# Optimization experiments

Measured on AMD Instinct MI355X. Metric: run time of the kernel, lower is better.

## Reference

```python
import jax, jax.numpy as jnp
import numpy as np

COUT, CIN = 1024, 1024  # self.shape = (cout, cin) in the torch module
NNZ = 131072


def setup_inputs() -> dict:
    key = jax.random.key(0)
    k_x, k_v, k_r, k_c = jax.random.split(key, 4)
    x = jax.random.normal(k_x, (4, 4096, CIN), dtype=jnp.float32)
    values = jax.random.normal(k_v, (NNZ,), dtype=jnp.float32)
    rows = jax.random.randint(k_r, (NNZ,), 0, COUT, dtype=jnp.int32)
    cols = jax.random.randint(k_c, (NNZ,), 0, CIN, dtype=jnp.int32)
    indices = jnp.stack([rows, cols], axis=0)  # [2, nnz], integer-valued
    return {"x": x, "values": values, "indices": indices}


def reference(x, values, indices):
    # torch: sparse_coo_tensor(indices, values, (cout, cin)).coalesce();
    # coalescing sums duplicate (row, col) entries -> scatter-add densify.
    rows, cols = indices[0], indices[1]
    W = jnp.zeros((COUT, CIN), dtype=values.dtype).at[rows, cols].add(values)
    # 3D path: out[b, l, co] = sum_ci W[co, ci] * x[b, l, ci]
    return jnp.einsum('blc,oc->blo', x, W)
```

## Files before the change

### kernel.cpp

```cpp
#include <hip/hip_runtime.h>
#include <cstdint>
#include <cstddef>

#define CIN  1024
#define COUT 1024

typedef __attribute__((ext_vector_type(8))) short bf16x8;
typedef __attribute__((ext_vector_type(4))) float f32x4;

__device__ __forceinline__ unsigned short f2bf(float f) {
    union { float f; unsigned int i; } v;
    v.f = f;
    unsigned int u = v.i;
    u += 0x7FFFu + ((u >> 16) & 1u);
    return (unsigned short)(u >> 16);
}

__device__ __forceinline__ void cvt8(const float* __restrict__ s,
                                     unsigned short* __restrict__ d) {
    float4 v0 = *(const float4*)s;
    float4 v1 = *(const float4*)(s + 4);
    union { bf16x8 v; unsigned short u[8]; } w;
    w.u[0] = f2bf(v0.x); w.u[1] = f2bf(v0.y); w.u[2] = f2bf(v0.z); w.u[3] = f2bf(v0.w);
    w.u[4] = f2bf(v1.x); w.u[5] = f2bf(v1.y); w.u[6] = f2bf(v1.z); w.u[7] = f2bf(v1.w);
    *(bf16x8*)d = w.v;
}

__global__ void zero_f32(float4* __restrict__ p) {
    p[blockIdx.x * 256 + threadIdx.x] = float4{0.f, 0.f, 0.f, 0.f};
}

__global__ void scatter_cvtx(const float* __restrict__ vals,
                             const int* __restrict__ rows,
                             const int* __restrict__ cols,
                             float* __restrict__ W, int nnz, int nsb,
                             const float* __restrict__ x,
                             unsigned short* __restrict__ Xb) {
    const int b = blockIdx.x;
    if (b < nsb) {
        const int i = b * 256 + threadIdx.x;
        if (i < nnz) atomicAdd(W + (size_t)rows[i] * CIN + cols[i], vals[i]);
    } else {
        const size_t i = (((size_t)(b - nsb) * 256) + threadIdx.x) * 8;
        cvt8(x + i, Xb + i);
    }
}

__global__ void cvt_bf16_bulk(const float* __restrict__ src, unsigned short* __restrict__ dst) {
    size_t i = ((size_t)blockIdx.x * 256 + threadIdx.x) * 8;
    cvt8(src + i, dst + i);
}


#define GLD16(SRC_, DST_)                                                     \
  __builtin_amdgcn_global_load_lds(                                           \
      (const __attribute__((address_space(1))) void*)(SRC_),                  \
      (__attribute__((address_space(3))) void*)(DST_), 16, 0, 0)

#define STAGE_A(BUF_, HALF_, KT_) do {                                        \
    GLD16(pa + (size_t)((HALF_) * 128)      * CIN + (size_t)(KT_) * 64,       \
          As + (BUF_) * 16384 + ((HALF_) * 128) * 64 + tid8);                 \
    GLD16(pa + (size_t)((HALF_) * 128 + 64) * CIN + (size_t)(KT_) * 64,       \
          As + (BUF_) * 16384 + ((HALF_) * 128 + 64) * 64 + tid8);            \
  } while (0)

#define STAGE_B(BUF_, HALF_, KT_) do {                                        \
    GLD16(pb + (size_t)((HALF_) * 128)      * CIN + (size_t)(KT_) * 64,       \
          Bs + (BUF_) * 16384 + ((HALF_) * 128) * 64 + tid8);                 \
    GLD16(pb + (size_t)((HALF_) * 128 + 64) * CIN + (size_t)(KT_) * 64,       \
          Bs + (BUF_) * 16384 + ((HALF_) * 128 + 64) * 64 + tid8);            \
  } while (0)

#define LOAD_A(BUF_, QA_) do {                                                \
    const unsigned short* ab_ = As + (BUF_) * 16384 + ((QA_) * 128 + wm64) * 64; \
    _Pragma("unroll")                                                         \
    for (int ks_ = 0; ks_ < 2; ++ks_) {                                       \
      const int cx_ = ((ks_ * 4 + quad) ^ s7) * 8;                            \
      _Pragma("unroll")                                                       \
      for (int mf_ = 0; mf_ < 4; ++mf_)                                       \
        af[ks_][mf_] = *(const bf16x8*)(ab_ + (mf_ * 16 + l16) * 64 + cx_);   \
    }                                                                         \
  } while (0)

#define LOAD_B(BUF_, QB_, DST_) do {                                          \
    const unsigned short* bb_ = Bs + (BUF_) * 16384 + ((QB_) * 128 + wn32) * 64; \
    _Pragma("unroll")                                                         \
    for (int ks_ = 0; ks_ < 2; ++ks_) {                                       \
      const int cx_ = ((ks_ * 4 + quad) ^ s7) * 8;                            \
      _Pragma("unroll")                                                       \
      for (int nf_ = 0; nf_ < 2; ++nf_)                                       \
        DST_[ks_][nf_] = *(const bf16x8*)(bb_ + (nf_ * 16 + l16) * 64 + cx_); \
    }                                                                         \
  } while (0)

#define MFMA_Q(QA_, QB_, BF_)                                                 \
    _Pragma("unroll")                                                         \
    for (int ks_ = 0; ks_ < 2; ++ks_)                                         \
      _Pragma("unroll")                                                       \
      for (int mf_ = 0; mf_ < 4; ++mf_)                                       \
        _Pragma("unroll")                                                     \
        for (int nf_ = 0; nf_ < 2; ++nf_)                                     \
          acc[QA_][QB_][mf_][nf_] = __builtin_amdgcn_mfma_f32_16x16x32_bf16(  \
              af[ks_][mf_], BF_[ks_][nf_], acc[QA_][QB_][mf_][nf_], 0, 0, 0)

#define WRITE_CQ(QA_, QB_) do {                                               \
    _Pragma("unroll")                                                         \
    for (int mf_ = 0; mf_ < 4; ++mf_)                                         \
      _Pragma("unroll")                                                       \
      for (int nf_ = 0; nf_ < 2; ++nf_) {                                     \
        const int row0_ = rowA0 + (QA_) * 128 + wm64 + mf_ * 16 + quad * 4;   \
        float* cp_ = C + (size_t)row0_ * COUT                                 \
                       + rowB0 + (QB_) * 128 + wn32 + nf_ * 16 + l16;         \
        _Pragma("unroll")                                                     \
        for (int r_ = 0; r_ < 4; ++r_)                                        \
            cp_[(size_t)r_ * COUT] = acc[QA_][QB_][mf_][nf_][r_];             \
      }                                                                       \
  } while (0)

#define SYNC_PRE() do {                                                       \
    __builtin_amdgcn_s_barrier();                                             \
    __builtin_amdgcn_s_setprio(1);                                            \
  } while (0)

#define SYNC_POST() __builtin_amdgcn_s_setprio(0)

__global__ __launch_bounds__(512, 2) void gemm_8ph_v4(
    const unsigned short* __restrict__ A,
    const unsigned short* __restrict__ B,
    float* __restrict__ C,
    int M) {
    (void)M;
    constexpr int K = CIN;

    __shared__ __align__(16) unsigned short As[2 * 16384];
    __shared__ __align__(16) unsigned short Bs[2 * 16384];

    const int tid  = threadIdx.x;
    const int lane = tid & 63;
    const int w    = tid >> 6;
    const int quad = lane >> 4;
    const int l16  = lane & 15;
    const int s7   = l16 & 7;
    const int wm64 = (w >> 2) * 64;
    const int wn32 = (w & 3) * 32;

    const int rowA0 = blockIdx.x * 256;
    const int rowB0 = blockIdx.y * 256;

    const int stg_row = tid >> 3;
    const int c_data  = (tid & 7) ^ (stg_row & 7);
    const int tid8    = tid * 8;
    const unsigned short* pa = A + (size_t)(rowA0 + stg_row) * K + c_data * 8;
    const unsigned short* pb = B + (size_t)(rowB0 + stg_row) * K + c_data * 8;

    f32x4 acc[2][2][4][2] = {};

    STAGE_A(0, 0, 0); STAGE_B(0, 0, 0); STAGE_B(0, 1, 0); STAGE_A(0, 1, 0);
    STAGE_A(1, 0, 1); STAGE_B(1, 0, 1);
    asm volatile("s_waitcnt vmcnt(4)" ::: "memory");
    __builtin_amdgcn_s_barrier();

#pragma unroll 1
    for (int i = 0; i < 7; ++i) {
        const int k1 = 2 * i + 1;
        const int k2 = 2 * i + 2;
        const int k3 = 2 * i + 3;

        bf16x8 af[2][4];
        bf16x8 bf0[2][2], bf1[2][2];

        LOAD_A(0, 0); LOAD_B(0, 0, bf0);
        STAGE_B(1, 1, k1);
        SYNC_PRE(); MFMA_Q(0, 0, bf0); SYNC_POST();
        __builtin_amdgcn_s_barrier();

        LOAD_B(0, 1, bf1);
        STAGE_A(1, 1, k1);
        SYNC_PRE(); MFMA_Q(0, 1, bf1); SYNC_POST();
        __builtin_amdgcn_s_barrier();

        LOAD_A(0, 1);
        STAGE_A(0, 0, k2);
        SYNC_PRE(); MFMA_Q(1, 0, bf0); SYNC_POST();
        __builtin_amdgcn_s_barrier();

        STAGE_B(0, 0, k2);
        SYNC_PRE(); MFMA_Q(1, 1, bf1); SYNC_POST();
        asm volatile("s_waitcnt vmcnt(4)" ::: "memory");
        __builtin_amdgcn_s_barrier();

        LOAD_A(1, 0); LOAD_B(1, 0, bf0);
        STAGE_B(0, 1, k2);
        SYNC_PRE(); MFMA_Q(0, 0, bf0); SYNC_POST();
        __builtin_amdgcn_s_barrier();

        LOAD_B(1, 1, bf1);
        STAGE_A(0, 1, k2);
        SYNC_PRE(); MFMA_Q(0, 1, bf1); SYNC_POST();
        __builtin_amdgcn_s_barrier();

        LOAD_A(1, 1);
        STAGE_A(1, 0, k3);
        SYNC_PRE(); MFMA_Q(1, 0, bf0); SYNC_POST();
        __builtin_amdgcn_s_barrier();

        STAGE_B(1, 0, k3);
        SYNC_PRE(); MFMA_Q(1, 1, bf1); SYNC_POST();
        asm volatile("s_waitcnt vmcnt(4)" ::: "memory");
        __builtin_amdgcn_s_barrier();
    }

    {
        bf16x8 af[2][4];
        bf16x8 bf0[2][2], bf1[2][2];

        LOAD_A(0, 0); LOAD_B(0, 0, bf0);
        STAGE_B(1, 1, 15);
        SYNC_PRE(); MFMA_Q(0, 0, bf0); SYNC_POST();
        __builtin_amdgcn_s_barrier();

        LOAD_B(0, 1, bf1);
        STAGE_A(1, 1, 15);
        SYNC_PRE(); MFMA_Q(0, 1, bf1); SYNC_POST();
        __builtin_amdgcn_s_barrier();

        LOAD_A(0, 1);
        SYNC_PRE(); MFMA_Q(1, 0, bf0); SYNC_POST();
        __builtin_amdgcn_s_barrier();

        SYNC_PRE(); MFMA_Q(1, 1, bf1); SYNC_POST();
        asm volatile("s_waitcnt vmcnt(0)" ::: "memory");
        __builtin_amdgcn_s_barrier();

        LOAD_A(1, 0); LOAD_B(1, 0, bf0); LOAD_B(1, 1, bf1);
        __builtin_amdgcn_s_setprio(1); MFMA_Q(0, 0, bf0); __builtin_amdgcn_s_setprio(0);
        WRITE_CQ(0, 0);

        __builtin_amdgcn_s_setprio(1); MFMA_Q(0, 1, bf1); __builtin_amdgcn_s_setprio(0);
        WRITE_CQ(0, 1);

        LOAD_A(1, 1);
        __builtin_amdgcn_s_setprio(1); MFMA_Q(1, 0, bf0); __builtin_amdgcn_s_setprio(0);
        WRITE_CQ(1, 0);

        __builtin_amdgcn_s_setprio(1); MFMA_Q(1, 1, bf1); __builtin_amdgcn_s_setprio(0);
        WRITE_CQ(1, 1);
    }
}

extern "C" void kernel_launch(void* const* d_in, const int* in_sizes, int n_in,
                              void* d_out, int out_size, void* d_ws, size_t ws_size,
                              hipStream_t stream) {
    const float* x    = (const float*)d_in[0];
    const float* vals = (const float*)d_in[1];
    const int*   idx  = (const int*)d_in[2];

    float* out = (float*)d_out;

    const int nnz = in_sizes[2] / 2;
    const int M   = in_sizes[0] / CIN;

    const size_t wf_bytes = (size_t)COUT * CIN * sizeof(float);
    const size_t wb_bytes = (size_t)COUT * CIN * sizeof(unsigned short);

    float*          Wf = (float*)d_ws;
    unsigned short* Wb = (unsigned short*)((char*)d_ws + wf_bytes);
    unsigned short* Xb = (unsigned short*)((char*)d_ws + wf_bytes + wb_bytes);

    const int nsb = (nnz + 255) / 256;
    const unsigned cvtx_blocks = (unsigned)((size_t)M * CIN / (256 * 8));

    zero_f32<<<dim3(COUT * CIN / (256 * 4)), dim3(256), 0, stream>>>((float4*)Wf);
    scatter_cvtx<<<dim3((unsigned)nsb + cvtx_blocks), dim3(256), 0, stream>>>(
        vals, idx, idx + nnz, Wf, nnz, nsb, x, Xb);
    cvt_bf16_bulk<<<dim3(COUT * CIN / (256 * 8)), dim3(256), 0, stream>>>(Wf, Wb);
    gemm_8ph_v4<<<dim3(M / 256, COUT / 256), dim3(512), 0, stream>>>(Xb, Wb, out, M);
}
```

Baseline: 155.0 us.

## Replace eight-phase interleaved GEMM pipeline with simple two-barrier double buffering

```diff
diff --git a/kernel.cpp b/kernel.cpp
--- a/kernel.cpp
+++ b/kernel.cpp
@@ -71,6 +71,11 @@
           Bs + (BUF_) * 16384 + ((HALF_) * 128 + 64) * 64 + tid8);            \
   } while (0)
 
+#define STAGE_TILE(BUF_, KT_) do {                                            \
+    STAGE_A(BUF_, 0, KT_); STAGE_A(BUF_, 1, KT_);                             \
+    STAGE_B(BUF_, 0, KT_); STAGE_B(BUF_, 1, KT_);                             \
+  } while (0)
+
 #define LOAD_A(BUF_, QA_) do {                                                \
     const unsigned short* ab_ = As + (BUF_) * 16384 + ((QA_) * 128 + wm64) * 64; \
     _Pragma("unroll")                                                         \
@@ -102,6 +107,19 @@
         for (int nf_ = 0; nf_ < 2; ++nf_)                                     \
           acc[QA_][QB_][mf_][nf_] = __builtin_amdgcn_mfma_f32_16x16x32_bf16(  \
               af[ks_][mf_], BF_[ks_][nf_], acc[QA_][QB_][mf_][nf_], 0, 0, 0)
+
+#define TILE_COMPUTE(BUF_) do {                                               \
+    bf16x8 af[2][4];                                                          \
+    bf16x8 bf0[2][2], bf1[2][2];                                              \
+    LOAD_A(BUF_, 0); LOAD_B(BUF_, 0, bf0); LOAD_B(BUF_, 1, bf1);              \
+    __builtin_amdgcn_s_setprio(1);                                            \
+    MFMA_Q(0, 0, bf0); MFMA_Q(0, 1, bf1);                                     \
+    __builtin_amdgcn_s_setprio(0);                                            \
+    LOAD_A(BUF_, 1);                                                          \
+    __builtin_amdgcn_s_setprio(1);                                            \
+    MFMA_Q(1, 0, bf0); MFMA_Q(1, 1, bf1);                                     \
+    __builtin_amdgcn_s_setprio(0);                                            \
+  } while (0)
 
 #define WRITE_CQ(QA_, QB_) do {                                               \
     _Pragma("unroll")                                                         \
@@ -117,14 +135,7 @@
       }                                                                       \
   } while (0)
 
-#define SYNC_PRE() do {                                                       \
-    __builtin_amdgcn_s_barrier();                                             \
-    __builtin_amdgcn_s_setprio(1);                                            \
-  } while (0)
-
-#define SYNC_POST() __builtin_amdgcn_s_setprio(0)
-
-__global__ __launch_bounds__(512, 2) void gemm_8ph_v4(
+__global__ __launch_bounds__(512, 2) void gemm_2bar(
     const unsigned short* __restrict__ A,
     const unsigned short* __restrict__ B,
     float* __restrict__ C,
@@ -155,83 +166,32 @@
 
     f32x4 acc[2][2][4][2] = {};
 
-    STAGE_A(0, 0, 0); STAGE_B(0, 0, 0); STAGE_B(0, 1, 0); STAGE_A(0, 1, 0);
-    STAGE_A(1, 0, 1); STAGE_B(1, 0, 1);
-    asm volatile("s_waitcnt vmcnt(4)" ::: "memory");
+    STAGE_TILE(0, 0);
+    STAGE_TILE(1, 1);
+    asm volatile("s_waitcnt vmcnt(8)" ::: "memory");
     __builtin_amdgcn_s_barrier();
 
 #pragma unroll 1
     for (int i = 0; i < 7; ++i) {
-        const int k1 = 2 * i + 1;
-        const int k2 = 2 * i + 2;
-        const int k3 = 2 * i + 3;
-
-        bf16x8 af[2][4];
-        bf16x8 bf0[2][2], bf1[2][2];
-
-        LOAD_A(0, 0); LOAD_B(0, 0, bf0);
-        STAGE_B(1, 1, k1);
-        SYNC_PRE(); MFMA_Q(0, 0, bf0); SYNC_POST();
-        __builtin_amdgcn_s_barrier();
-
-        LOAD_B(0, 1, bf1);
-        STAGE_A(1, 1, k1);
-        SYNC_PRE(); MFMA_Q(0, 1, bf1); SYNC_POST();
-        __builtin_amdgcn_s_barrier();
-
-        LOAD_A(0, 1);
-        STAGE_A(0, 0, k2);
-        SYNC_PRE(); MFMA_Q(1, 0, bf0); SYNC_POST();
-        __builtin_amdgcn_s_barrier();
-
-        STAGE_B(0, 0, k2);
-        SYNC_PRE(); MFMA_Q(1, 1, bf1); SYNC_POST();
-        asm volatile("s_waitcnt vmcnt(4)" ::: "memory");
-        __builtin_amdgcn_s_barrier();
-
-        LOAD_A(1, 0); LOAD_B(1, 0, bf0);
-        STAGE_B(0, 1, k2);
-        SYNC_PRE(); MFMA_Q(0, 0, bf0); SYNC_POST();
-        __builtin_amdgcn_s_barrier();
-
-        LOAD_B(1, 1, bf1);
-        STAGE_A(0, 1, k2);
-        SYNC_PRE(); MFMA_Q(0, 1, bf1); SYNC_POST();
-        __builtin_amdgcn_s_barrier();
-
-        LOAD_A(1, 1);
-        STAGE_A(1, 0, k3);
-        SYNC_PRE(); MFMA_Q(1, 0, bf0); SYNC_POST();
-        __builtin_amdgcn_s_barrier();
-
-        STAGE_B(1, 0, k3);
-        SYNC_PRE(); MFMA_Q(1, 1, bf1); SYNC_POST();
-        asm volatile("s_waitcnt vmcnt(4)" ::: "memory");
+        TILE_COMPUTE(0);
+        __builtin_amdgcn_s_barrier();
+        STAGE_TILE(0, 2 * i + 2);
+        asm volatile("s_waitcnt vmcnt(8)" ::: "memory");
+        __builtin_amdgcn_s_barrier();
+        TILE_COMPUTE(1);
+        __builtin_amdgcn_s_barrier();
+        STAGE_TILE(1, 2 * i + 3);
+        asm volatile("s_waitcnt vmcnt(8)" ::: "memory");
         __builtin_amdgcn_s_barrier();
     }
+
+    TILE_COMPUTE(0);
+    asm volatile("s_waitcnt vmcnt(0)" ::: "memory");
+    __builtin_amdgcn_s_barrier();
 
     {
         bf16x8 af[2][4];
         bf16x8 bf0[2][2], bf1[2][2];
-
-        LOAD_A(0, 0); LOAD_B(0, 0, bf0);
-        STAGE_B(1, 1, 15);
-        SYNC_PRE(); MFMA_Q(0, 0, bf0); SYNC_POST();
-        __builtin_amdgcn_s_barrier();
-
-        LOAD_B(0, 1, bf1);
-        STAGE_A(1, 1, 15);
-        SYNC_PRE(); MFMA_Q(0, 1, bf1); SYNC_POST();
-        __builtin_amdgcn_s_barrier();
-
-        LOAD_A(0, 1);
-        SYNC_PRE(); MFMA_Q(1, 0, bf0); SYNC_POST();
-        __builtin_amdgcn_s_barrier();
-
-        SYNC_PRE(); MFMA_Q(1, 1, bf1); SYNC_POST();
-        asm volatile("s_waitcnt vmcnt(0)" ::: "memory");
-        __builtin_amdgcn_s_barrier();
-
         LOAD_A(1, 0); LOAD_B(1, 0, bf0); LOAD_B(1, 1, bf1);
         __builtin_amdgcn_s_setprio(1); MFMA_Q(0, 0, bf0); __builtin_amdgcn_s_setprio(0);
         WRITE_CQ(0, 0);
@@ -274,5 +234,5 @@
     scatter_cvtx<<<dim3((unsigned)nsb + cvtx_blocks), dim3(256), 0, stream>>>(
         vals, idx, idx + nnz, Wf, nnz, nsb, x, Xb);
     cvt_bf16_bulk<<<dim3(COUT * CIN / (256 * 8)), dim3(256), 0, stream>>>(Wf, Wb);
-    gemm_8ph_v4<<<dim3(M / 256, COUT / 256), dim3(512), 0, stream>>>(Xb, Wb, out, M);
-}
+    gemm_2bar<<<dim3(M / 256, COUT / 256), dim3(512), 0, stream>>>(Xb, Wb, out, M);
+}
```

New measurement: 156.0 us. No clear change (+0.7%).
